# Optimization experiments

Measured on AMD Instinct MI355X. Metric: run time of the kernel, lower is better.

## Reference

```python
import jax, jax.numpy as jnp
import numpy as np

B, N, D, H = 2, 2048, 1024, 16
HD = D // H

def setup_inputs() -> dict:
    key = jax.random.key(0)
    ks = jax.random.split(key, 8)
    s = lambda fan_in: 1.0 / np.sqrt(fan_in)
    return {
        "x": jax.random.normal(ks[0], (B, N, D), jnp.float32),
        "coverage": jax.random.uniform(ks[1], (B, N, 1), jnp.float32),
        "w_qkv": jax.random.normal(ks[2], (D, 3 * D), jnp.float32) * s(D),
        "w_out": jax.random.normal(ks[3], (D, D), jnp.float32) * s(D),
        "b_out": jnp.zeros((D,), jnp.float32),
        "w_ce1": jax.random.normal(ks[4], (1, D // 4), jnp.float32),
        "b_ce1": jnp.zeros((D // 4,), jnp.float32),
        "w_ce2": jax.random.normal(ks[5], (D // 4, H), jnp.float32) * s(D // 4),
        "b_ce2": jnp.zeros((H,), jnp.float32),
        "w_fg1": jax.random.normal(ks[6], (D, D // 4), jnp.float32) * s(D),
        "b_fg1": jnp.zeros((D // 4,), jnp.float32),
        "w_fg2": jax.random.normal(ks[7], (D // 4, 1), jnp.float32) * s(D // 4),
        "b_fg2": jnp.zeros((1,), jnp.float32),
    }

def reference(x, coverage, w_qkv, w_out, b_out, w_ce1, b_ce1, w_ce2, b_ce2,
              w_fg1, b_fg1, w_fg2, b_fg2):
    b, n, d = x.shape
    h = w_ce2.shape[1]
    hd = d // h
    scale = hd ** -0.5
    qkv = x @ w_qkv  # (B,N,3D)
    q, k, v = jnp.split(qkv, 3, axis=-1)
    q = q.reshape(b, n, h, hd).transpose(0, 2, 1, 3)  # (B,H,N,hd)
    k = k.reshape(b, n, h, hd).transpose(0, 2, 1, 3)
    v = v.reshape(b, n, h, hd).transpose(0, 2, 1, 3)
    attn = jnp.einsum("bhnd,bhmd->bhnm", q, k) * scale  # (B,H,N,N)
    # coverage bias: MLP(1 -> D/4 -> H), broadcast over query dim
    cov = jax.nn.silu(coverage @ w_ce1 + b_ce1) @ w_ce2 + b_ce2  # (B,N,H)
    cov_bias = cov.transpose(0, 2, 1)[:, :, None, :]  # (B,H,1,N)
    # fusion gate on mean-pooled features
    x_pooled = x.mean(axis=1)  # (B,D)
    g = jax.nn.sigmoid(jax.nn.silu(x_pooled @ w_fg1 + b_fg1) @ w_fg2 + b_fg2)  # (B,1)
    g = g[:, :, None, None]  # (B,1,1,1)
    # g*(attn+bias) + (1-g)*attn == attn + g*bias (exact same math)
    attn = attn + g * cov_bias
    attn = jax.nn.softmax(attn, axis=-1)
    out = jnp.einsum("bhnm,bhmd->bhnd", attn, v)  # (B,H,N,hd)
    out = out.transpose(0, 2, 1, 3).reshape(b, n, d)
    return out @ w_out + b_out
```

## Files before the change

kernel.cpp:

```cpp
#include <hip/hip_runtime.h>
#include <math.h>

typedef __bf16 bf16_t;
typedef __bf16 bf16x8 __attribute__((ext_vector_type(8)));
typedef __bf16 bf16x4 __attribute__((ext_vector_type(4)));
typedef float f32x4 __attribute__((ext_vector_type(4)));

#define MFMA16(a, b, c) __builtin_amdgcn_mfma_f32_16x16x32_bf16((a), (b), (c), 0, 0, 0)

constexpr int Bc = 2, Nc = 2048, Dc = 1024, Hc = 16, HDc = 64;
constexpr float C1 = 0.18033688011112042f;
constexpr float LOG2E = 1.4426950408889634f;

__device__ __forceinline__ void glds16(const bf16_t* g, bf16_t* l) {
    __builtin_amdgcn_global_load_lds(
        (const __attribute__((address_space(1))) unsigned int*)g,
        (__attribute__((address_space(3))) unsigned int*)l, 16, 0, 0);
}

__global__ __launch_bounds__(256) void prep_all(const float* __restrict__ x,
                                                const float* __restrict__ w_qkv,
                                                const float* __restrict__ w_out,
                                                const float* __restrict__ coverage,
                                                const float* __restrict__ w_ce1,
                                                const float* __restrict__ b_ce1,
                                                const float* __restrict__ w_ce2,
                                                const float* __restrict__ b_ce2,
                                                bf16_t* __restrict__ Xb,
                                                bf16_t* __restrict__ Wt,
                                                bf16_t* __restrict__ WoT,
                                                float* __restrict__ pooled,
                                                float* __restrict__ biasbuf) {
    __shared__ bf16_t tile[64 * 66];
    int blk = blockIdx.x, t = threadIdx.x;
    if (blk < 512) {
        int row0 = blk * 8;
        int b = row0 >> 11;
        int c = t * 4;
        float s0 = 0.f, s1 = 0.f, s2 = 0.f, s3 = 0.f;
#pragma unroll
        for (int rr = 0; rr < 8; ++rr) {
            size_t off = (size_t)(row0 + rr) * 1024 + c;
            float4 v = *(const float4*)(x + off);
            bf16x4 o = { (bf16_t)v.x, (bf16_t)v.y, (bf16_t)v.z, (bf16_t)v.w };
            *(bf16x4*)(Xb + off) = o;
            s0 += v.x; s1 += v.y; s2 += v.z; s3 += v.w;
        }
        atomicAdd(&pooled[b * 1024 + c + 0], s0);
        atomicAdd(&pooled[b * 1024 + c + 1], s1);
        atomicAdd(&pooled[b * 1024 + c + 2], s2);
        atomicAdd(&pooled[b * 1024 + c + 3], s3);
    } else if (blk < 1536) {
        int idx = blk - 512;
        int cx = idx & 63, ry = idx >> 6;
        const float* src; bf16_t* dst; int C;
        if (cx < 48) { src = w_qkv; dst = Wt; C = 3072; }
        else         { src = w_out; dst = WoT; C = 1024; cx -= 48; }
        const int R = 1024;
        int r0 = ry * 64, c0 = cx * 64;
        int cl = t & 63, rl = t >> 6;
#pragma unroll
        for (int p = 0; p < 16; ++p) {
            int r = p * 4 + rl;
            tile[r * 66 + cl] = (bf16_t)src[(size_t)(r0 + r) * C + c0 + cl];
        }
        __syncthreads();
#pragma unroll
        for (int p = 0; p < 16; ++p) {
            int r = p * 4 + rl;
            dst[(size_t)(c0 + r) * R + r0 + cl] = tile[cl * 66 + r];
        }
    } else {
        int cb = blk - 1536;
        int h = t & 15;
        int gn = cb * 16 + (t >> 4);
        int b = gn >> 11, n = gn & 2047;
        float c = coverage[gn];
        float acc = b_ce2[h];
        for (int j = 0; j < 256; ++j) {
            float tv = c * w_ce1[j] + b_ce1[j];
            tv = tv / (1.0f + __expf(-tv));
            acc += tv * w_ce2[j * 16 + h];
        }
        biasbuf[((size_t)b * 16 + h) * 2048 + n] = LOG2E * acc;
    }
}

__global__ __launch_bounds__(256) void gate1(const float* __restrict__ pooled,
                                             const float* __restrict__ w_fg1,
                                             const float* __restrict__ b_fg1,
                                             const float* __restrict__ w_fg2,
                                             float* __restrict__ hacc) {
    int b = blockIdx.x >> 8, j = blockIdx.x & 255;
    int t = threadIdx.x;
    float p = 0.f;
#pragma unroll
    for (int i = 0; i < 4; ++i) {
        int d = t * 4 + i;
        p += pooled[b * 1024 + d] * w_fg1[d * 256 + j];
    }
#pragma unroll
    for (int off = 32; off > 0; off >>= 1) p += __shfl_down(p, off);
    __shared__ float red[4];
    if ((t & 63) == 0) red[t >> 6] = p;
    __syncthreads();
    if (t == 0) {
        float hj = (red[0] + red[1] + red[2] + red[3]) * (1.0f / 2048.0f) + b_fg1[j];
        hj = hj / (1.0f + __expf(-hj));
        atomicAdd(&hacc[b], hj * w_fg2[j]);
    }
}

__global__ __launch_bounds__(256) void qkv_gemm(const bf16_t* __restrict__ Xb,
                                                const bf16_t* __restrict__ Wt,
                                                bf16_t* __restrict__ Q,
                                                bf16_t* __restrict__ Kb,
                                                bf16_t* __restrict__ Vt) {
    __shared__ __align__(16) bf16_t At[128 * 64];
    __shared__ __align__(16) bf16_t Bt[128 * 64];
    int t = threadIdx.x, w = t >> 6, lane = t & 63;
    int l16 = lane & 15, quad = lane >> 4;
    int wm = w & 1, wx = w >> 1;
    int m0 = blockIdx.x * 128;
    int n0 = blockIdx.y * 128;
    f32x4 acc[4][4] = {};
    int swl = l16 & 7;

    for (int k0 = 0; k0 < 1024; k0 += 64) {
#pragma unroll
        for (int i = 0; i < 4; ++i) {
            int fb = i * 4096 + w * 1024;
            int f = fb + lane * 16;
            int row = f >> 7;
            int ch = (f >> 4) & 7;
            int sc = ch ^ (row & 7);
            glds16(Wt + (size_t)(n0 + row) * 1024 + k0 + sc * 8, At + (fb >> 1));
            glds16(Xb + (size_t)(m0 + row) * 1024 + k0 + sc * 8, Bt + (fb >> 1));
        }
        __syncthreads();
#pragma unroll
        for (int s = 0; s < 2; ++s) {
            bf16x8 afr[4], bfr[4];
#pragma unroll
            for (int mi = 0; mi < 4; ++mi)
                afr[mi] = *(const bf16x8*)(At + (wm * 64 + mi * 16 + l16) * 64 + (((s * 4 + quad) ^ swl) * 8));
#pragma unroll
            for (int ni = 0; ni < 4; ++ni)
                bfr[ni] = *(const bf16x8*)(Bt + (wx * 64 + ni * 16 + l16) * 64 + (((s * 4 + quad) ^ swl) * 8));
#pragma unroll
            for (int mi = 0; mi < 4; ++mi)
#pragma unroll
                for (int ni = 0; ni < 4; ++ni)
                    acc[mi][ni] = MFMA16(afr[mi], bfr[ni], acc[mi][ni]);
        }
        __syncthreads();
    }

    int sec = n0 >> 10;
#pragma unroll
    for (int mi = 0; mi < 4; ++mi) {
        int gc = n0 + wm * 64 + mi * 16 + quad * 4;
        int dcol = gc & 1023;
        int h = dcol >> 6, hd = dcol & 63;
#pragma unroll
        for (int ni = 0; ni < 4; ++ni) {
            int gx = m0 + wx * 64 + ni * 16 + l16;
            int b = gx >> 11, n = gx & 2047;
            size_t bh = (size_t)(b * 16 + h);
            if (sec == 2) {
                int np = (n & ~31) + ((n >> 2) & 3) * 8 + ((n >> 4) & 1) * 4 + (n & 3);
#pragma unroll
                for (int r = 0; r < 4; ++r)
                    Vt[(bh * 64 + hd + r) * 2048 + np] = (bf16_t)acc[mi][ni][r];
            } else {
                bf16x4 pk = { (bf16_t)acc[mi][ni][0], (bf16_t)acc[mi][ni][1],
                              (bf16_t)acc[mi][ni][2], (bf16_t)acc[mi][ni][3] };
                bf16_t* dst = (sec == 0 ? Q : Kb);
                *(bf16x4*)(dst + (bh * 2048 + n) * 64 + hd) = pk;
            }
        }
    }
}

__global__ __launch_bounds__(256) void attn_k(const bf16_t* __restrict__ Q,
                                              const bf16_t* __restrict__ Kb,
                                              const bf16_t* __restrict__ Vt,
                                              const float* __restrict__ biasbuf,
                                              const float* __restrict__ hacc,
                                              const float* __restrict__ b_fg2,
                                              bf16_t* __restrict__ O) {
    __shared__ __align__(16) bf16_t kbuf[2][64 * 64];
    __shared__ __align__(16) bf16_t vbuf[2][64 * 64];
    int t = threadIdx.x, w = t >> 6, lane = t & 63;
    int l16 = lane & 15, quad = lane >> 4;
    int bh = blockIdx.y;
    int b = bh >> 4, h = bh & 15;
    int qa = blockIdx.x * 128 + w * 32;
    const bf16_t* Qh = Q + (size_t)bh * 2048 * 64;
    const bf16_t* Kh = Kb + (size_t)bh * 2048 * 64;
    const bf16_t* Vh = Vt + (size_t)bh * 64 * 2048;
    const float* bih = biasbuf + (size_t)bh * 2048;
    float gate = 1.0f / (1.0f + __expf(-(hacc[b] + b_fg2[0])));

    int fb0 = w * 2048, fb1 = fb0 + 1024;
    int f0 = fb0 + lane * 16, f1 = fb1 + lane * 16;
    int krow0 = f0 >> 7, kch0 = ((f0 >> 4) & 7) ^ (krow0 & 7);
    int krow1 = f1 >> 7, kch1 = ((f1 >> 4) & 7) ^ (krow1 & 7);

    bf16x8 qf[2][2];
#pragma unroll
    for (int g = 0; g < 2; ++g)
#pragma unroll
        for (int dh = 0; dh < 2; ++dh)
            qf[g][dh] = *(const bf16x8*)(Qh + (size_t)(qa + g * 16 + l16) * 64 + dh * 32 + quad * 8);

    f32x4 o[2][4] = {};
    f32x4 osum[2] = {};
    const f32x4 zero = { 0.f, 0.f, 0.f, 0.f };
    int swl = l16 & 7;
    bf16x8 ones;
#pragma unroll
    for (int i = 0; i < 8; ++i) ones[i] = (bf16_t)1.0f;

    {
        glds16(Kh + (size_t)krow0 * 64 + kch0 * 8, &kbuf[0][fb0 >> 1]);
        glds16(Kh + (size_t)krow1 * 64 + kch1 * 8, &kbuf[0][fb1 >> 1]);
        glds16(Vh + (size_t)krow0 * 2048 + kch0 * 8, &vbuf[0][fb0 >> 1]);
        glds16(Vh + (size_t)krow1 * 2048 + kch1 * 8, &vbuf[0][fb1 >> 1]);
    }

    for (int it = 0; it < 32; ++it) {
        int j0 = it * 64, sel = it & 1;
        __syncthreads();
        if (it + 1 < 32) {
            int jn = j0 + 64, sn = sel ^ 1;
            glds16(Kh + (size_t)(jn + krow0) * 64 + kch0 * 8, &kbuf[sn][fb0 >> 1]);
            glds16(Kh + (size_t)(jn + krow1) * 64 + kch1 * 8, &kbuf[sn][fb1 >> 1]);
            glds16(Vh + (size_t)krow0 * 2048 + jn + kch0 * 8, &vbuf[sn][fb0 >> 1]);
            glds16(Vh + (size_t)krow1 * 2048 + jn + kch1 * 8, &vbuf[sn][fb1 >> 1]);
        }
        const bf16_t* kb = kbuf[sel];
        const bf16_t* vb = vbuf[sel];

        float4 bias[4];
#pragma unroll
        for (int kt = 0; kt < 4; ++kt) {
            bias[kt] = *(const float4*)(bih + j0 + kt * 16 + quad * 4);
            bias[kt].x *= gate; bias[kt].y *= gate;
            bias[kt].z *= gate; bias[kt].w *= gate;
        }

        f32x4 s[4][2];
#pragma unroll
        for (int kt = 0; kt < 4; ++kt) {
            bf16x8 kf0 = *(const bf16x8*)(kb + (kt * 16 + l16) * 64 + ((quad ^ swl) * 8));
            bf16x8 kf1 = *(const bf16x8*)(kb + (kt * 16 + l16) * 64 + (((4 + quad) ^ swl) * 8));
#pragma unroll
            for (int g = 0; g < 2; ++g) {
                s[kt][g] = MFMA16(kf0, qf[g][0], zero);
                s[kt][g] = MFMA16(kf1, qf[g][1], s[kt][g]);
            }
        }

#pragma unroll
        for (int kt = 0; kt < 4; ++kt) {
            const float* bp = (const float*)&bias[kt];
#pragma unroll
            for (int g = 0; g < 2; ++g)
#pragma unroll
                for (int r = 0; r < 4; ++r)
                    s[kt][g][r] = __builtin_amdgcn_exp2f(s[kt][g][r] * C1 + bp[r]);
        }

        bf16x8 pf[2][2];
#pragma unroll
        for (int g = 0; g < 2; ++g)
#pragma unroll
            for (int pv = 0; pv < 2; ++pv) {
                bf16x8 tmp;
#pragma unroll
                for (int i = 0; i < 4; ++i) {
                    tmp[i]     = (bf16_t)s[2 * pv][g][i];
                    tmp[i + 4] = (bf16_t)s[2 * pv + 1][g][i];
                }
                pf[g][pv] = tmp;
            }

#pragma unroll
        for (int dt = 0; dt < 4; ++dt) {
            const bf16_t* vrow = vb + (dt * 16 + l16) * 64;
#pragma unroll
            for (int pv = 0; pv < 2; ++pv) {
                bf16x8 vf = *(const bf16x8*)(vrow + (((pv * 4 + quad) ^ swl) * 8));
#pragma unroll
                for (int g = 0; g < 2; ++g)
                    o[g][dt] = MFMA16(pf[g][pv], vf, o[g][dt]);
            }
        }
#pragma unroll
        for (int g = 0; g < 2; ++g) {
            osum[g] = MFMA16(pf[g][0], ones, osum[g]);
            osum[g] = MFMA16(pf[g][1], ones, osum[g]);
        }
    }

#pragma unroll
    for (int g = 0; g < 2; ++g) {
        float rinv[4];
#pragma unroll
        for (int r = 0; r < 4; ++r) rinv[r] = 1.0f / osum[g][r];
#pragma unroll
        for (int dt = 0; dt < 4; ++dt)
#pragma unroll
            for (int r = 0; r < 4; ++r) {
                int row = qa + g * 16 + quad * 4 + r;
                O[(size_t)(b * 2048 + row) * 1024 + h * 64 + dt * 16 + l16] =
                    (bf16_t)(o[g][dt][r] * rinv[r]);
            }
    }
}

__global__ __launch_bounds__(256) void out_gemm(const bf16_t* __restrict__ A,
                                                const bf16_t* __restrict__ Wt,
                                                const float* __restrict__ bias,
                                                float* __restrict__ Cout) {
    __shared__ __align__(16) bf16_t At[64 * 64];
    __shared__ __align__(16) bf16_t Bt[128 * 64];
    int t = threadIdx.x, w = t >> 6, lane = t & 63;
    int l16 = lane & 15, quad = lane >> 4;
    int wm = w & 1, wx = w >> 1;
    int m0 = blockIdx.x * 128;
    int n0 = blockIdx.y * 64;
    f32x4 acc[2][4] = {};
    int swl = l16 & 7;

    for (int k0 = 0; k0 < 1024; k0 += 64) {
#pragma unroll
        for (int i = 0; i < 2; ++i) {
            int fb = i * 4096 + w * 1024;
            int f = fb + lane * 16;
            int row = f >> 7;
            int ch = (f >> 4) & 7;
            int sc = ch ^ (row & 7);
            glds16(Wt + (size_t)(n0 + row) * 1024 + k0 + sc * 8, At + (fb >> 1));
        }
#pragma unroll
        for (int i = 0; i < 4; ++i) {
            int fb = i * 4096 + w * 1024;
            int f = fb + lane * 16;
            int row = f >> 7;
            int ch = (f >> 4) & 7;
            int sc = ch ^ (row & 7);
            glds16(A + (size_t)(m0 + row) * 1024 + k0 + sc * 8, Bt + (fb >> 1));
        }
        __syncthreads();
#pragma unroll
        for (int s = 0; s < 2; ++s) {
            bf16x8 afr[2], bfr[4];
#pragma unroll
            for (int mi = 0; mi < 2; ++mi)
                afr[mi] = *(const bf16x8*)(At + (wm * 32 + mi * 16 + l16) * 64 + (((s * 4 + quad) ^ swl) * 8));
#pragma unroll
            for (int ni = 0; ni < 4; ++ni)
                bfr[ni] = *(const bf16x8*)(Bt + (wx * 64 + ni * 16 + l16) * 64 + (((s * 4 + quad) ^ swl) * 8));
#pragma unroll
            for (int mi = 0; mi < 2; ++mi)
#pragma unroll
                for (int ni = 0; ni < 4; ++ni)
                    acc[mi][ni] = MFMA16(afr[mi], bfr[ni], acc[mi][ni]);
        }
        __syncthreads();
    }

#pragma unroll
    for (int mi = 0; mi < 2; ++mi) {
        int gc = n0 + wm * 32 + mi * 16 + quad * 4;
        float4 bv = *(const float4*)(bias + gc);
#pragma unroll
        for (int ni = 0; ni < 4; ++ni) {
            int gx = m0 + wx * 64 + ni * 16 + l16;
            float4 ov = { acc[mi][ni][0] + bv.x, acc[mi][ni][1] + bv.y,
                          acc[mi][ni][2] + bv.z, acc[mi][ni][3] + bv.w };
            *(float4*)(Cout + (size_t)gx * 1024 + gc) = ov;
        }
    }
}

extern "C" void kernel_launch(void* const* d_in, const int* in_sizes, int n_in,
                              void* d_out, int out_size, void* d_ws, size_t ws_size,
                              hipStream_t stream) {
    const float* x     = (const float*)d_in[0];
    const float* cov   = (const float*)d_in[1];
    const float* w_qkv = (const float*)d_in[2];
    const float* w_out = (const float*)d_in[3];
    const float* b_out = (const float*)d_in[4];
    const float* w_ce1 = (const float*)d_in[5];
    const float* b_ce1 = (const float*)d_in[6];
    const float* w_ce2 = (const float*)d_in[7];
    const float* b_ce2 = (const float*)d_in[8];
    const float* w_fg1 = (const float*)d_in[9];
    const float* b_fg1 = (const float*)d_in[10];
    const float* w_fg2 = (const float*)d_in[11];
    const float* b_fg2 = (const float*)d_in[12];

    char* ws = (char*)d_ws;
    bf16_t* Wt     = (bf16_t*)(ws);
    bf16_t* WoT    = (bf16_t*)(ws + 6291456);
    bf16_t* Xb     = (bf16_t*)(ws + 8388608);
    bf16_t* Qb     = (bf16_t*)(ws + 16777216);
    bf16_t* Kbb    = (bf16_t*)(ws + 25165824);
    bf16_t* Vt     = (bf16_t*)(ws + 33554432);
    bf16_t* Ob     = (bf16_t*)(ws + 41943040);
    float*  pooled = (float*)(ws + 50331648);
    float*  hacc   = (float*)(ws + 50339840);
    float*  biasb  = (float*)(ws + 50340096);

    hipMemsetAsync(pooled, 0, 8192 + 256, stream);
    prep_all<<<1792, 256, 0, stream>>>(x, w_qkv, w_out, cov, w_ce1, b_ce1, w_ce2, b_ce2,
                                       Xb, Wt, WoT, pooled, biasb);
    gate1<<<512, 256, 0, stream>>>(pooled, w_fg1, b_fg1, w_fg2, hacc);
    qkv_gemm<<<dim3(32, 24), 256, 0, stream>>>(Xb, Wt, Qb, Kbb, Vt);
    attn_k<<<dim3(16, 32), 256, 0, stream>>>(Qb, Kbb, Vt, biasb, hacc, b_fg2, Ob);
    out_gemm<<<dim3(32, 16), 256, 0, stream>>>(Ob, WoT, b_out, (float*)d_out);
}
```

Baseline: 281.8 us.

## Split V projection into transposed GEMM with vectorized stores; pre-apply gate to bias

The V third of the QKV projection moves into its own GEMM kernel whose operand roles are swapped, so each lane holds four consecutive tokens and can write the transposed V layout as packed bf16x4 stores instead of scattered scalar stores. Q and K stay in a reduced GEMM. The gate sigmoid and its multiply on the coverage bias move into a small separate kernel, so the attention loop no longer scales the bias on every tile. This adds two kernel launches and one extra pass over the bias buffer, and the GEMM work is now split across two smaller grids.

```diff
diff --git a/kernel.cpp b/kernel.cpp
--- a/kernel.cpp
+++ b/kernel.cpp
@@ -111,11 +111,21 @@
     }
 }
 
-__global__ __launch_bounds__(256) void qkv_gemm(const bf16_t* __restrict__ Xb,
-                                                const bf16_t* __restrict__ Wt,
-                                                bf16_t* __restrict__ Q,
-                                                bf16_t* __restrict__ Kb,
-                                                bf16_t* __restrict__ Vt) {
+__global__ __launch_bounds__(256) void gatebias(float* __restrict__ biasbuf,
+                                                const float* __restrict__ hacc,
+                                                const float* __restrict__ b_fg2) {
+    int idx = (blockIdx.x * 256 + threadIdx.x) * 4;
+    int b = idx >> 15;
+    float g = 1.0f / (1.0f + __expf(-(hacc[b] + b_fg2[0])));
+    float4 v = *(const float4*)(biasbuf + idx);
+    v.x *= g; v.y *= g; v.z *= g; v.w *= g;
+    *(float4*)(biasbuf + idx) = v;
+}
+
+__global__ __launch_bounds__(256) void qk_gemm(const bf16_t* __restrict__ Xb,
+                                               const bf16_t* __restrict__ Wt,
+                                               bf16_t* __restrict__ Q,
+                                               bf16_t* __restrict__ Kb) {
     __shared__ __align__(16) bf16_t At[128 * 64];
     __shared__ __align__(16) bf16_t Bt[128 * 64];
     int t = threadIdx.x, w = t >> 6, lane = t & 63;
@@ -157,6 +167,7 @@
     }
 
     int sec = n0 >> 10;
+    bf16_t* dst = (sec == 0 ? Q : Kb);
 #pragma unroll
     for (int mi = 0; mi < 4; ++mi) {
         int gc = n0 + wm * 64 + mi * 16 + quad * 4;
@@ -167,17 +178,69 @@
             int gx = m0 + wx * 64 + ni * 16 + l16;
             int b = gx >> 11, n = gx & 2047;
             size_t bh = (size_t)(b * 16 + h);
-            if (sec == 2) {
-                int np = (n & ~31) + ((n >> 2) & 3) * 8 + ((n >> 4) & 1) * 4 + (n & 3);
-#pragma unroll
-                for (int r = 0; r < 4; ++r)
-                    Vt[(bh * 64 + hd + r) * 2048 + np] = (bf16_t)acc[mi][ni][r];
-            } else {
-                bf16x4 pk = { (bf16_t)acc[mi][ni][0], (bf16_t)acc[mi][ni][1],
-                              (bf16_t)acc[mi][ni][2], (bf16_t)acc[mi][ni][3] };
-                bf16_t* dst = (sec == 0 ? Q : Kb);
-                *(bf16x4*)(dst + (bh * 2048 + n) * 64 + hd) = pk;
-            }
+            bf16x4 pk = { (bf16_t)acc[mi][ni][0], (bf16_t)acc[mi][ni][1],
+                          (bf16_t)acc[mi][ni][2], (bf16_t)acc[mi][ni][3] };
+            *(bf16x4*)(dst + (bh * 2048 + n) * 64 + hd) = pk;
+        }
+    }
+}
+
+__global__ __launch_bounds__(256) void v_gemm(const bf16_t* __restrict__ Xb,
+                                              const bf16_t* __restrict__ Wt,
+                                              bf16_t* __restrict__ Vt) {
+    __shared__ __align__(16) bf16_t At[128 * 64];
+    __shared__ __align__(16) bf16_t Bt[128 * 64];
+    int t = threadIdx.x, w = t >> 6, lane = t & 63;
+    int l16 = lane & 15, quad = lane >> 4;
+    int wm = w & 1, wx = w >> 1;
+    int n0 = blockIdx.x * 128;
+    int m0 = blockIdx.y * 128;
+    const bf16_t* WtV = Wt + (size_t)2048 * 1024;
+    f32x4 acc[4][4] = {};
+    int swl = l16 & 7;
+
+    for (int k0 = 0; k0 < 1024; k0 += 64) {
+#pragma unroll
+        for (int i = 0; i < 4; ++i) {
+            int fb = i * 4096 + w * 1024;
+            int f = fb + lane * 16;
+            int row = f >> 7;
+            int ch = (f >> 4) & 7;
+            int sc = ch ^ (row & 7);
+            glds16(Xb + (size_t)(m0 + row) * 1024 + k0 + sc * 8, At + (fb >> 1));
+            glds16(WtV + (size_t)(n0 + row) * 1024 + k0 + sc * 8, Bt + (fb >> 1));
+        }
+        __syncthreads();
+#pragma unroll
+        for (int s = 0; s < 2; ++s) {
+            bf16x8 afr[4], bfr[4];
+#pragma unroll
+            for (int mi = 0; mi < 4; ++mi)
+                afr[mi] = *(const bf16x8*)(At + (wm * 64 + mi * 16 + l16) * 64 + (((s * 4 + quad) ^ swl) * 8));
+#pragma unroll
+            for (int ni = 0; ni < 4; ++ni)
+                bfr[ni] = *(const bf16x8*)(Bt + (wx * 64 + ni * 16 + l16) * 64 + (((s * 4 + quad) ^ swl) * 8));
+#pragma unroll
+            for (int mi = 0; mi < 4; ++mi)
+#pragma unroll
+                for (int ni = 0; ni < 4; ++ni)
+                    acc[mi][ni] = MFMA16(afr[mi], bfr[ni], acc[mi][ni]);
+        }
+        __syncthreads();
+    }
+
+#pragma unroll
+    for (int mi = 0; mi < 4; ++mi) {
+        int rowx = m0 + wm * 64 + mi * 16 + quad * 4;
+        int b = rowx >> 11, n = rowx & 2047;
+        int np = (n & ~31) + ((n >> 2) & 3) * 8 + ((n >> 4) & 1) * 4;
+#pragma unroll
+        for (int ni = 0; ni < 4; ++ni) {
+            int colv = n0 + wx * 64 + ni * 16 + l16;
+            int h = colv >> 6, hd = colv & 63;
+            bf16x4 pk = { (bf16_t)acc[mi][ni][0], (bf16_t)acc[mi][ni][1],
+                          (bf16_t)acc[mi][ni][2], (bf16_t)acc[mi][ni][3] };
+            *(bf16x4*)(Vt + ((size_t)(b * 16 + h) * 64 + hd) * 2048 + np) = pk;
         }
     }
 }
@@ -186,8 +249,6 @@
                                               const bf16_t* __restrict__ Kb,
                                               const bf16_t* __restrict__ Vt,
                                               const float* __restrict__ biasbuf,
-                                              const float* __restrict__ hacc,
-                                              const float* __restrict__ b_fg2,
                                               bf16_t* __restrict__ O) {
     __shared__ __align__(16) bf16_t kbuf[2][64 * 64];
     __shared__ __align__(16) bf16_t vbuf[2][64 * 64];
@@ -200,7 +261,6 @@
     const bf16_t* Kh = Kb + (size_t)bh * 2048 * 64;
     const bf16_t* Vh = Vt + (size_t)bh * 64 * 2048;
     const float* bih = biasbuf + (size_t)bh * 2048;
-    float gate = 1.0f / (1.0f + __expf(-(hacc[b] + b_fg2[0])));
 
     int fb0 = w * 2048, fb1 = fb0 + 1024;
     int f0 = fb0 + lane * 16, f1 = fb1 + lane * 16;
@@ -244,11 +304,8 @@
 
         float4 bias[4];
 #pragma unroll
-        for (int kt = 0; kt < 4; ++kt) {
+        for (int kt = 0; kt < 4; ++kt)
             bias[kt] = *(const float4*)(bih + j0 + kt * 16 + quad * 4);
-            bias[kt].x *= gate; bias[kt].y *= gate;
-            bias[kt].z *= gate; bias[kt].w *= gate;
-        }
 
         f32x4 s[4][2];
 #pragma unroll
@@ -419,7 +476,9 @@
     prep_all<<<1792, 256, 0, stream>>>(x, w_qkv, w_out, cov, w_ce1, b_ce1, w_ce2, b_ce2,
                                        Xb, Wt, WoT, pooled, biasb);
     gate1<<<512, 256, 0, stream>>>(pooled, w_fg1, b_fg1, w_fg2, hacc);
-    qkv_gemm<<<dim3(32, 24), 256, 0, stream>>>(Xb, Wt, Qb, Kbb, Vt);
-    attn_k<<<dim3(16, 32), 256, 0, stream>>>(Qb, Kbb, Vt, biasb, hacc, b_fg2, Ob);
+    gatebias<<<64, 256, 0, stream>>>(biasb, hacc, b_fg2);
+    qk_gemm<<<dim3(32, 16), 256, 0, stream>>>(Xb, Wt, Qb, Kbb);
+    v_gemm<<<dim3(8, 32), 256, 0, stream>>>(Xb, Wt, Vt);
+    attn_k<<<dim3(16, 32), 256, 0, stream>>>(Qb, Kbb, Vt, biasb, Ob);
     out_gemm<<<dim3(32, 16), 256, 0, stream>>>(Ob, WoT, b_out, (float*)d_out);
 }
```

Measured after the change: 280.2 us. Within noise of the previous version (-0.6%).
